# Optimization experiments

Hardware: AMD Instinct MI355X
Metric: run time of the kernel (lower is better)

The kernel has to match this reference:

```python
import jax, jax.numpy as jnp
import numpy as np

EPS = 1e-5

def _layer_norm(x, gamma, beta):
    # LayerNorm over the last two dims [C, 128], matching nn.LayerNorm([C, 128])
    mean = jnp.mean(x, axis=(-2, -1), keepdims=True)
    var = jnp.var(x, axis=(-2, -1), keepdims=True)
    return (x - mean) * jax.lax.rsqrt(var + EPS) * gamma + beta


def setup_inputs() -> dict:
    key = jax.random.key(0)
    ks = jax.random.split(key, 7)
    B, C, N, L = 64, 1024, 128, 512
    W_SCALE = 0.02  # keep pre-softmax logits / activations in a sane range
    return {
        "X_in": jax.random.normal(ks[0], (B, C, N), jnp.float32),
        "T": jax.random.normal(ks[1], (B, C, L), jnp.float32),
        "Wq": jax.random.normal(ks[2], (C, C), jnp.float32) * W_SCALE,
        "Wk": jax.random.normal(ks[3], (C, C), jnp.float32) * W_SCALE,
        "Wv": jax.random.normal(ks[4], (C, C), jnp.float32) * W_SCALE,
        "Wf1": jax.random.normal(ks[5], (C, C), jnp.float32) * W_SCALE,
        "Wf2": jax.random.normal(ks[6], (C, C), jnp.float32) * W_SCALE,
        "gamma": jnp.ones((C, N), jnp.float32),
        "beta": jnp.zeros((C, N), jnp.float32),
    }


def reference(X_in, T, Wq, Wk, Wv, Wf1, Wf2, gamma, beta):
    C = Wq.shape[1]  # feature_map_cs (intended value of the buggy X_in.weight.shape[1])
    # 1x1 Conv1d == per-position channel matmul: weight [out, in]
    q = jnp.einsum('oc,bcn->bon', Wq, X_in)      # [B, C, N]
    k = jnp.einsum('oc,bcl->bol', Wk, T)         # [B, C, L]
    sim = jnp.einsum('bcn,bcl->bnl', q, k) / jnp.sqrt(jnp.float32(C))  # [B, N, L]
    attn = jax.nn.softmax(sim, axis=2)           # softmax over tokens L
    v = jnp.einsum('oc,bcl->bol', Wv, T)         # [B, C, L]
    ctx = jnp.einsum('bcl,bnl->bcn', v, attn)    # [B, C, N] == bmm(values, attn^T)
    X_out = _layer_norm(X_in + ctx, gamma, beta)
    h = jax.nn.relu(jnp.einsum('oc,bcn->bon', Wf1, X_out))
    ffn = jnp.einsum('oc,bcn->bon', Wf2, h)
    return _layer_norm(X_out + ffn, gamma, beta)
```

## Files before the change

kernel.cpp:

```cpp
#include <hip/hip_runtime.h>


using bf16   = __bf16;
using bf16x4 = __attribute__((ext_vector_type(4))) __bf16;
using bf16x8 = __attribute__((ext_vector_type(8))) __bf16;
using f32x4  = __attribute__((ext_vector_type(4))) float;

static constexpr int  Bb = 64;
static constexpr int  Cc = 1024;
static constexpr int  Nn = 128;
static constexpr int  Ll = 512;
static constexpr long long PLANE = (long long)Cc * Nn;
static constexpr float INV_PLANE = 1.0f / 131072.0f;

__device__ __forceinline__ void gload_lds16(const void* g, void* l) {
    __builtin_amdgcn_global_load_lds(
        (__attribute__((address_space(1))) void*)g,
        (__attribute__((address_space(3))) void*)l,
        16, 0, 0);
}

__global__ void __launch_bounds__(256)
prep_all(const float* __restrict__ Wv, const float* __restrict__ Wf1,
         const float* __restrict__ Wf2, const float* __restrict__ Wq,
         const float* __restrict__ Wk, const float* __restrict__ X,
         const float* __restrict__ T,
         bf16* __restrict__ WvB, bf16* __restrict__ Wf1B, bf16* __restrict__ Wf2B,
         bf16* __restrict__ WqT, bf16* __restrict__ WkT,
         bf16* __restrict__ Xt, bf16* __restrict__ Tt, bf16* __restrict__ Tb) {
    __shared__ float tile[64][65];
    const int bx = blockIdx.x;
    const int t  = threadIdx.x;
    if (bx < 3072) {
        const float* in = bx < 1024 ? Wv : (bx < 2048 ? Wf1 : Wf2);
        bf16* out       = bx < 1024 ? WvB : (bx < 2048 ? Wf1B : Wf2B);
        int i = (bx & 1023) * 256 + t;
        float4 v = reinterpret_cast<const float4*>(in)[i];
        bf16x4 o = { (bf16)v.x, (bf16)v.y, (bf16)v.z, (bf16)v.w };
        reinterpret_cast<bf16x4*>(out)[i] = o;
        return;
    }
    const float* in; bf16* outT; bf16* outS = nullptr;
    int R, S, bxx, byy, bz = 0;
    if (bx < 3584) {
        int j = bx - 3072;
        in = (j >= 256) ? Wk : Wq; outT = (j >= 256) ? WkT : WqT;
        R = Cc; S = Cc; j &= 255; bxx = j & 15; byy = j >> 4;
    } else if (bx < 5632) {
        int j = bx - 3584; bz = j >> 5; j &= 31;
        bxx = j & 1; byy = j >> 1; in = X; outT = Xt; R = Cc; S = Nn;
    } else {
        int j = bx - 5632; bz = j >> 7; j &= 127;
        bxx = j & 7; byy = j >> 3; in = T; outT = Tt; outS = Tb; R = Cc; S = Ll;
    }
    long long plane = (long long)R * S;
    in   += (long long)bz * plane;
    outT += (long long)bz * plane;
    if (outS) outS += (long long)bz * plane;
    int s0 = bxx * 64, r0 = byy * 64;
    int rl = t >> 4;
    int sc = (t & 15) * 4;
    #pragma unroll
    for (int p = 0; p < 4; ++p) {
        int r = p * 16 + rl;
        float4 v = *(const float4*)(in + (long long)(r0 + r) * S + s0 + sc);
        *(float4*)&tile[r][sc] = v;
        if (outS) {
            bf16x4 o = { (bf16)v.x, (bf16)v.y, (bf16)v.z, (bf16)v.w };
            *(bf16x4*)(outS + (long long)(r0 + r) * S + s0 + sc) = o;
        }
    }
    __syncthreads();
    long long tb = ((long long)(s0 >> 6) * (R >> 6) + (r0 >> 6)) * 4096;
    int sb = t >> 3;
    int rg = (t & 7) * 8;
    #pragma unroll
    for (int p = 0; p < 2; ++p) {
        int s = sb + p * 32;
        bf16x8 o;
        #pragma unroll
        for (int j = 0; j < 8; ++j) o[j] = (bf16)tile[rg + j][s];
        *(bf16x8*)(outT + tb + s * 64 + rg) = o;
    }
}

#define GEMM_PROLOGUE_AND_LOOP(A_, Bt_, K_, TA_, TB_)                              \
    __shared__ bf16 As[2][128 * 64];                                               \
    __shared__ bf16 Bs[2][128 * 64];                                               \
    const int n0   = blockIdx.x * 128;                                             \
    const int m0   = blockIdx.y * 128;                                             \
    const int t    = threadIdx.x;                                                  \
    const int lane = t & 63;                                                       \
    const int w    = t >> 6;                                                       \
    const int wr   = (w >> 1) * 64;                                                \
    const int wc   = (w & 1) * 64;                                                 \
    const int lr   = lane & 15;                                                    \
    const int hi4  = (lane >> 4) * 16;                                             \
    const int sw   = (lr & 7) << 4;                                                \
    const int stepA_ = (TA_) ? 4096 : 64;                                          \
    const int stepB_ = (TB_) ? 4096 : 64;                                          \
    const bf16* gA[4]; const bf16* gB[4]; int lo[4];                               \
    _Pragma("unroll")                                                              \
    for (int p = 0; p < 4; ++p) {                                                  \
        int o = w * 1024 + lane * 16 + p * 4096;                                   \
        int row = o >> 7;                                                          \
        int scol = ((o & 127) ^ ((row & 7) << 4)) >> 1;                            \
        lo[p] = o;                                                                 \
        int ra = m0 + row, rb = n0 + row;                                          \
        gA[p] = (TA_) ? A_ + ((long long)(ra >> 6) * (K_ >> 6)) * 4096             \
                           + (ra & 63) * 64 + scol                                 \
                      : A_ + (long long)ra * K_ + scol;                            \
        gB[p] = (TB_) ? Bt_ + ((long long)(rb >> 6) * (K_ >> 6)) * 4096            \
                            + (rb & 63) * 64 + scol                                \
                      : Bt_ + (long long)rb * K_ + scol;                           \
    }                                                                              \
    f32x4 acc[4][4] = {};                                                          \
    const int NT_ = K_ / 64;                                                       \
    _Pragma("unroll")                                                              \
    for (int p = 0; p < 4; ++p) gload_lds16(gA[p], (char*)As[0] + lo[p]);          \
    _Pragma("unroll")                                                              \
    for (int p = 0; p < 4; ++p) gload_lds16(gB[p], (char*)Bs[0] + lo[p]);          \
    __syncthreads();                                                               \
    int cur_ = 0;                                                                  \
    for (int kt = 0; kt < NT_; ++kt) {                                             \
        if (kt + 1 < NT_) {                                                        \
            _Pragma("unroll")                                                      \
            for (int p = 0; p < 4; ++p)                                            \
                gload_lds16(gA[p] + (long long)(kt + 1) * stepA_,                  \
                            (char*)As[cur_ ^ 1] + lo[p]);                          \
            _Pragma("unroll")                                                      \
            for (int p = 0; p < 4; ++p)                                            \
                gload_lds16(gB[p] + (long long)(kt + 1) * stepB_,                  \
                            (char*)Bs[cur_ ^ 1] + lo[p]);                          \
        }                                                                          \
        const bf16* As_ = As[cur_]; const bf16* Bs_ = Bs[cur_];                    \
        _Pragma("unroll")                                                          \
        for (int kk = 0; kk < 2; ++kk) {                                           \
            bf16x8 af[4], bfr[4];                                                  \
            _Pragma("unroll")                                                      \
            for (int i = 0; i < 4; ++i) {                                          \
                int ra = wr + i * 16 + lr;                                         \
                int rb = wc + i * 16 + lr;                                         \
                af[i]  = *(const bf16x8*)((const char*)As_ +                       \
                          ((((ra << 7) + (kk << 6) + hi4)) ^ sw));                 \
                bfr[i] = *(const bf16x8*)((const char*)Bs_ +                       \
                          ((((rb << 7) + (kk << 6) + hi4)) ^ sw));                 \
            }                                                                      \
            _Pragma("unroll")                                                      \
            for (int mi = 0; mi < 4; ++mi)                                         \
                _Pragma("unroll")                                                  \
                for (int ni = 0; ni < 4; ++ni)                                     \
                    acc[mi][ni] = __builtin_amdgcn_mfma_f32_16x16x32_bf16(         \
                        af[mi], bfr[ni], acc[mi][ni], 0, 0, 0);                    \
        }                                                                          \
        __syncthreads();                                                           \
        cur_ ^= 1;                                                                 \
    }

template <typename OutT, bool RELU, int TA, int TB>
__global__ void __launch_bounds__(256, 2)
gemm_tn(const bf16* __restrict__ A, const bf16* __restrict__ Bt, OutT* __restrict__ C,
        int M, int N, int K, long long sA, long long sBt, long long sC, float scale) {
    A  += (long long)blockIdx.z * sA;
    Bt += (long long)blockIdx.z * sBt;
    C  += (long long)blockIdx.z * sC;
    GEMM_PROLOGUE_AND_LOOP(A, Bt, K, TA, TB)
    const int rbase = m0 + wr + (lane >> 4) * 4;
    const int cbase = n0 + wc + lr;
    #pragma unroll
    for (int mi = 0; mi < 4; ++mi)
        #pragma unroll
        for (int ni = 0; ni < 4; ++ni)
            #pragma unroll
            for (int r = 0; r < 4; ++r) {
                float v = acc[mi][ni][r] * scale;
                if (RELU) v = fmaxf(v, 0.0f);
                C[(long long)(rbase + mi * 16 + r) * N + (cbase + ni * 16)] = (OutT)v;
            }
}

__global__ void __launch_bounds__(256, 2)
gemm_sim_exp(const bf16* __restrict__ A , const bf16* __restrict__ Bt ,
             bf16* __restrict__ E, float* __restrict__ rspart, int K,
             long long sA, long long sBt) {
    A  += (long long)blockIdx.z * sA;
    Bt += (long long)blockIdx.z * sBt;
    E  += (long long)blockIdx.z * ((long long)Nn * Ll);
    GEMM_PROLOGUE_AND_LOOP(A, Bt, K, 0, 1)
    const int rbase = m0 + wr + (lane >> 4) * 4;
    const int cbase = n0 + wc + lr;
    __shared__ float rs[2][128];
    float psum[4][4];
    #pragma unroll
    for (int mi = 0; mi < 4; ++mi)
        #pragma unroll
        for (int r = 0; r < 4; ++r) psum[mi][r] = 0.f;
    #pragma unroll
    for (int mi = 0; mi < 4; ++mi)
        #pragma unroll
        for (int ni = 0; ni < 4; ++ni)
            #pragma unroll
            for (int r = 0; r < 4; ++r) {
                float ev = __expf(acc[mi][ni][r] * 0.03125f);
                E[(long long)(rbase + mi * 16 + r) * Ll + (cbase + ni * 16)] = (bf16)ev;
                psum[mi][r] += ev;
            }
    #pragma unroll
    for (int mi = 0; mi < 4; ++mi)
        #pragma unroll
        for (int r = 0; r < 4; ++r) {
            float v = psum[mi][r];
            v += __shfl_xor(v, 1); v += __shfl_xor(v, 2);
            v += __shfl_xor(v, 4); v += __shfl_xor(v, 8);
            psum[mi][r] = v;
        }
    if (lr == 0) {
        #pragma unroll
        for (int mi = 0; mi < 4; ++mi)
            #pragma unroll
            for (int r = 0; r < 4; ++r)
                rs[wc ? 1 : 0][wr + (lane >> 4) * 4 + mi * 16 + r] = psum[mi][r];
    }
    __syncthreads();
    if (t < 128)
        rspart[((long long)blockIdx.z * 4 + blockIdx.x) * 128 + t] = rs[0][t] + rs[1][t];
}

__global__ void __launch_bounds__(256, 2)
gemm_u_scaled(const bf16* __restrict__ A , const bf16* __restrict__ Bt ,
              bf16* __restrict__ C, const float* __restrict__ rspart, int K,
              long long sA, long long sBt, long long sC) {
    A  += (long long)blockIdx.z * sA;
    Bt += (long long)blockIdx.z * sBt;
    C  += (long long)blockIdx.z * sC;
    const float* rp = rspart + (long long)blockIdx.z * 512;
    GEMM_PROLOGUE_AND_LOOP(A, Bt, K, 0, 0)
    const int rbase = m0 + wr + (lane >> 4) * 4;
    const int cbase = n0 + wc + lr;
    #pragma unroll
    for (int mi = 0; mi < 4; ++mi)
        #pragma unroll
        for (int r = 0; r < 4; ++r) {
            int row = rbase + mi * 16 + r;
            float inv = 1.f / (rp[row] + rp[128 + row] + rp[256 + row] + rp[384 + row]);
            #pragma unroll
            for (int ni = 0; ni < 4; ++ni)
                C[(long long)row * Cc + (cbase + ni * 16)] = (bf16)(acc[mi][ni][r] * inv);
        }
}

__global__ void __launch_bounds__(256, 2)
gemm_ctx_ln1(const bf16* __restrict__ A , const bf16* __restrict__ Bt ,
             const float* __restrict__ X, bf16* __restrict__ Z1, float* __restrict__ partials,
             int K, long long sBt) {
    const int N = Nn;
    Bt += (long long)blockIdx.z * sBt;
    X  += (long long)blockIdx.z * PLANE;
    Z1 += (long long)blockIdx.z * PLANE;
    GEMM_PROLOGUE_AND_LOOP(A, Bt, K, 0, 0)
    const int rbase = m0 + wr + (lane >> 4) * 4;
    const int cbase = n0 + wc + lr;
    float s = 0.f, ss = 0.f;
    #pragma unroll
    for (int mi = 0; mi < 4; ++mi)
        #pragma unroll
        for (int ni = 0; ni < 4; ++ni)
            #pragma unroll
            for (int r = 0; r < 4; ++r) {
                long long idx = (long long)(rbase + mi * 16 + r) * N + (cbase + ni * 16);
                float zv = acc[mi][ni][r] + X[idx];
                Z1[idx] = (bf16)zv;
                s += zv; ss += zv * zv;
            }
    #pragma unroll
    for (int off = 32; off; off >>= 1) { s += __shfl_xor(s, off); ss += __shfl_xor(ss, off); }
    __shared__ float red[8];
    if (lane == 0) { red[w] = s; red[4 + w] = ss; }
    __syncthreads();
    if (t == 0) {
        float S = red[0] + red[1] + red[2] + red[3];
        float SS = red[4] + red[5] + red[6] + red[7];
        float* p = partials + ((long long)blockIdx.z * 8 + blockIdx.y) * 2;
        p[0] = S; p[1] = SS;
    }
}

__global__ void __launch_bounds__(256, 2)
gemm_ffn_ln2(const bf16* __restrict__ A , const bf16* __restrict__ Bt ,
             const bf16* __restrict__ Z1, const float* __restrict__ pp1,
             const float* __restrict__ gamma, const float* __restrict__ beta,
             bf16* __restrict__ Z2, float* __restrict__ partials,
             int K, long long sA) {
    A  += (long long)blockIdx.z * sA;
    Z1 += (long long)blockIdx.z * PLANE;
    Z2 += (long long)blockIdx.z * PLANE;
    float S1 = 0.f, SS1 = 0.f;
    #pragma unroll
    for (int j = 0; j < 8; ++j) {
        S1  += pp1[((long long)blockIdx.z * 8 + j) * 2];
        SS1 += pp1[((long long)blockIdx.z * 8 + j) * 2 + 1];
    }
    const float mean1 = S1 * INV_PLANE;
    const float rstd1 = rsqrtf(SS1 * INV_PLANE - mean1 * mean1 + 1e-5f);
    GEMM_PROLOGUE_AND_LOOP(A, Bt, K, 0, 0)
    const int rbase = m0 + wr + (lane >> 4) * 4;
    const int cbase = n0 + wc + lr;
    float s = 0.f, ss = 0.f;
    #pragma unroll
    for (int mi = 0; mi < 4; ++mi)
        #pragma unroll
        for (int ni = 0; ni < 4; ++ni) {
            long long a = (long long)(cbase + ni * 16) * Nn + rbase + mi * 16;
            bf16x4 z1v = *(const bf16x4*)(Z1 + a);
            float4 g  = *(const float4*)(gamma + a);
            float4 be = *(const float4*)(beta + a);
            float x0 = ((float)z1v[0] - mean1) * rstd1 * g.x + be.x;
            float x1 = ((float)z1v[1] - mean1) * rstd1 * g.y + be.y;
            float x2 = ((float)z1v[2] - mean1) * rstd1 * g.z + be.z;
            float x3 = ((float)z1v[3] - mean1) * rstd1 * g.w + be.w;
            float z0 = acc[mi][ni][0] + x0, z1 = acc[mi][ni][1] + x1;
            float z2 = acc[mi][ni][2] + x2, z3 = acc[mi][ni][3] + x3;
            bf16x4 zo = { (bf16)z0, (bf16)z1, (bf16)z2, (bf16)z3 };
            *(bf16x4*)(Z2 + a) = zo;
            s  += z0 + z1 + z2 + z3;
            ss += z0 * z0 + z1 * z1 + z2 * z2 + z3 * z3;
        }
    #pragma unroll
    for (int off = 32; off; off >>= 1) { s += __shfl_xor(s, off); ss += __shfl_xor(ss, off); }
    __shared__ float red[8];
    if (lane == 0) { red[w] = s; red[4 + w] = ss; }
    __syncthreads();
    if (t == 0) {
        float S = red[0] + red[1] + red[2] + red[3];
        float SS = red[4] + red[5] + red[6] + red[7];
        float* p = partials + ((long long)blockIdx.z * 8 + blockIdx.x) * 2;
        p[0] = S; p[1] = SS;
    }
}

__global__ void ln1_norm_transpose(const bf16* __restrict__ Z1, const float* __restrict__ partials,
                                   const float* __restrict__ gamma, const float* __restrict__ beta,
                                   bf16* __restrict__ XoutT) {
    int b = blockIdx.z;
    float S = 0.f, SS = 0.f;
    #pragma unroll
    for (int j = 0; j < 8; ++j) {
        S  += partials[((long long)b * 8 + j) * 2];
        SS += partials[((long long)b * 8 + j) * 2 + 1];
    }
    float mean = S * INV_PLANE;
    float var  = SS * INV_PLANE - mean * mean;
    float rstd = rsqrtf(var + 1e-5f);
    __shared__ float tile[64][65];
    long long base = (long long)b * PLANE;
    int n0 = blockIdx.x * 64, c0 = blockIdx.y * 64;
    int t = threadIdx.x;
    int rl = t >> 4;
    int sc = (t & 15) * 4;
    #pragma unroll
    for (int p = 0; p < 4; ++p) {
        int r = p * 16 + rl;
        long long idx = (long long)(c0 + r) * Nn + n0 + sc;
        bf16x4 z  = *(const bf16x4*)(Z1 + base + idx);
        float4 g  = *(const float4*)(gamma + idx);
        float4 be = *(const float4*)(beta + idx);
        float4 o = {((float)z[0] - mean) * rstd * g.x + be.x,
                    ((float)z[1] - mean) * rstd * g.y + be.y,
                    ((float)z[2] - mean) * rstd * g.z + be.z,
                    ((float)z[3] - mean) * rstd * g.w + be.w};
        *(float4*)&tile[r][sc] = o;
    }
    __syncthreads();
    long long tb = ((long long)(n0 >> 6) * (Cc >> 6) + (c0 >> 6)) * 4096;
    int sb = t >> 3;
    int rg = (t & 7) * 8;
    #pragma unroll
    for (int p = 0; p < 2; ++p) {
        int n = sb + p * 32;
        bf16x8 o;
        #pragma unroll
        for (int j = 0; j < 8; ++j) o[j] = (bf16)tile[rg + j][n];
        *(bf16x8*)(XoutT + base + tb + n * 64 + rg) = o;
    }
}

__global__ void ln2_final(const bf16* __restrict__ Z2, const float* __restrict__ partials,
                          const float* __restrict__ gamma, const float* __restrict__ beta,
                          float* __restrict__ out) {
    int b = blockIdx.y;
    float S = 0.f, SS = 0.f;
    #pragma unroll
    for (int j = 0; j < 8; ++j) {
        S  += partials[((long long)b * 8 + j) * 2];
        SS += partials[((long long)b * 8 + j) * 2 + 1];
    }
    float mean = S * INV_PLANE;
    float var  = SS * INV_PLANE - mean * mean;
    float rstd = rsqrtf(var + 1e-5f);
    long long base = (long long)b * PLANE;
    int i = (blockIdx.x * 256 + threadIdx.x) * 8;
    bf16x8 z = *(const bf16x8*)(Z2 + base + i);
    #pragma unroll
    for (int h = 0; h < 2; ++h) {
        float4 g  = *(const float4*)(gamma + i + h * 4);
        float4 be = *(const float4*)(beta + i + h * 4);
        float4 o = {((float)z[h * 4 + 0] - mean) * rstd * g.x + be.x,
                    ((float)z[h * 4 + 1] - mean) * rstd * g.y + be.y,
                    ((float)z[h * 4 + 2] - mean) * rstd * g.z + be.z,
                    ((float)z[h * 4 + 3] - mean) * rstd * g.w + be.w};
        *(float4*)(out + base + i + h * 4) = o;
    }
}

extern "C" void kernel_launch(void* const* d_in, const int* in_sizes, int n_in,
                              void* d_out, int out_size, void* d_ws, size_t ws_size,
                              hipStream_t stream) {
    const float* X   = (const float*)d_in[0];
    const float* T   = (const float*)d_in[1];
    const float* Wq  = (const float*)d_in[2];
    const float* Wk  = (const float*)d_in[3];
    const float* Wv  = (const float*)d_in[4];
    const float* Wf1 = (const float*)d_in[5];
    const float* Wf2 = (const float*)d_in[6];
    const float* gamma = (const float*)d_in[7];
    const float* beta  = (const float*)d_in[8];
    float* out = (float*)d_out;
    char* ws = (char*)d_ws;
    const size_t MB = 1ull << 20;

    bf16* WvB  = (bf16*)(ws + 0 * MB);
    bf16* Wf1B = (bf16*)(ws + 2 * MB);
    bf16* Wf2B = (bf16*)(ws + 4 * MB);
    bf16* WqT  = (bf16*)(ws + 6 * MB);
    bf16* WkT  = (bf16*)(ws + 8 * MB);
    bf16* G2   = (bf16*)(ws + 10 * MB);
    bf16* Xt   = (bf16*)(ws + 12 * MB);
    bf16* Tt   = (bf16*)(ws + 28 * MB);
    bf16* Z1   = (bf16*)(ws + 28 * MB);
    bf16* Tb   = (bf16*)(ws + 92 * MB);
    bf16* XoutT= (bf16*)(ws + 92 * MB);
    bf16* hT   = (bf16*)(ws + 108 * MB);
    bf16* e    = (bf16*)(ws + 156 * MB);
    bf16* Z2   = (bf16*)(ws + 156 * MB);
    bf16* E    = (bf16*)(ws + 188 * MB);
    bf16* u    = (bf16*)(ws + 196 * MB);
    float* pp1 = (float*)(ws + 212 * MB);
    float* pp2 = (float*)(ws + 212 * MB + 65536);
    float* rsp = (float*)(ws + 213 * MB);

    dim3 blk256(256);

    prep_all<<<dim3(13824), blk256, 0, stream>>>(
        Wv, Wf1, Wf2, Wq, Wk, X, T, WvB, Wf1B, Wf2B, WqT, WkT, Xt, Tt, Tb);

    gemm_tn<bf16, false, 1, 1><<<dim3(8, 8, 1), blk256, 0, stream>>>(
        WkT, WqT, G2, Cc, Cc, Cc, 0, 0, 0, 1.f);
    gemm_tn<bf16, false, 1, 0><<<dim3(8, 1, Bb), blk256, 0, stream>>>(
        Xt, G2, e, Nn, Cc, Cc, (long long)Nn * Cc, 0, (long long)Nn * Cc, 1.f);
    gemm_sim_exp<<<dim3(4, 1, Bb), blk256, 0, stream>>>(
        e, Tt, E, rsp, Cc, (long long)Nn * Cc, (long long)Ll * Cc);
    gemm_u_scaled<<<dim3(8, 1, Bb), blk256, 0, stream>>>(
        E, Tb, u, rsp, Ll, (long long)Nn * Ll, (long long)Cc * Ll, (long long)Nn * Cc);
    gemm_ctx_ln1<<<dim3(1, 8, Bb), blk256, 0, stream>>>(
        WvB, u, X, Z1, pp1, Cc, (long long)Nn * Cc);
    ln1_norm_transpose<<<dim3(Nn / 64, Cc / 64, Bb), blk256, 0, stream>>>(
        Z1, pp1, gamma, beta, XoutT);
    gemm_tn<bf16, true, 1, 0><<<dim3(8, 1, Bb), blk256, 0, stream>>>(
        XoutT, Wf1B, hT, Nn, Cc, Cc, (long long)Nn * Cc, 0, (long long)Nn * Cc, 1.f);
    gemm_ffn_ln2<<<dim3(8, 1, Bb), blk256, 0, stream>>>(
        hT, Wf2B, Z1, pp1, gamma, beta, Z2, pp2, Cc, (long long)Nn * Cc);
    ln2_final<<<dim3(64, Bb), blk256, 0, stream>>>(Z2, pp2, gamma, beta, out);
}
```

Measured before the change: 293.3 us.

## Fuse T fp32-to-bf16 conversion into attention GEMMs and split-K the G2 GEMM

Drops the separate pass that converted T into transposed and plain bf16 copies. The sim and context GEMMs now read fp32 T directly, converting it in registers (through an LDS transpose for the sim GEMM) while staging tiles. This removes a large write-then-read of bf16 T through HBM. The Wk^T·Wq GEMM is also split four ways along K into fp32 partials plus a small reduce kernel, giving it more blocks to run on. The cost is twice the global read bytes for T in each GEMM, extra LDS and sync work inside the main loops, and one extra kernel launch.

```diff
diff --git a/kernel.cpp b/kernel.cpp
--- a/kernel.cpp
+++ b/kernel.cpp
@@ -24,10 +24,8 @@
 prep_all(const float* __restrict__ Wv, const float* __restrict__ Wf1,
          const float* __restrict__ Wf2, const float* __restrict__ Wq,
          const float* __restrict__ Wk, const float* __restrict__ X,
-         const float* __restrict__ T,
          bf16* __restrict__ WvB, bf16* __restrict__ Wf1B, bf16* __restrict__ Wf2B,
-         bf16* __restrict__ WqT, bf16* __restrict__ WkT,
-         bf16* __restrict__ Xt, bf16* __restrict__ Tt, bf16* __restrict__ Tb) {
+         bf16* __restrict__ WqT, bf16* __restrict__ WkT, bf16* __restrict__ Xt) {
     __shared__ float tile[64][65];
     const int bx = blockIdx.x;
     const int t  = threadIdx.x;
@@ -40,40 +38,30 @@
         reinterpret_cast<bf16x4*>(out)[i] = o;
         return;
     }
-    const float* in; bf16* outT; bf16* outS = nullptr;
+    const float* in; bf16* outT;
     int R, S, bxx, byy, bz = 0;
     if (bx < 3584) {
         int j = bx - 3072;
         in = (j >= 256) ? Wk : Wq; outT = (j >= 256) ? WkT : WqT;
         R = Cc; S = Cc; j &= 255; bxx = j & 15; byy = j >> 4;
-    } else if (bx < 5632) {
+    } else {
         int j = bx - 3584; bz = j >> 5; j &= 31;
         bxx = j & 1; byy = j >> 1; in = X; outT = Xt; R = Cc; S = Nn;
-    } else {
-        int j = bx - 5632; bz = j >> 7; j &= 127;
-        bxx = j & 7; byy = j >> 3; in = T; outT = Tt; outS = Tb; R = Cc; S = Ll;
     }
     long long plane = (long long)R * S;
     in   += (long long)bz * plane;
     outT += (long long)bz * plane;
-    if (outS) outS += (long long)bz * plane;
     int s0 = bxx * 64, r0 = byy * 64;
-    int rl = t >> 4;
-    int sc = (t & 15) * 4;
+    int rl = t >> 4, sc = (t & 15) * 4;
     #pragma unroll
     for (int p = 0; p < 4; ++p) {
         int r = p * 16 + rl;
         float4 v = *(const float4*)(in + (long long)(r0 + r) * S + s0 + sc);
         *(float4*)&tile[r][sc] = v;
-        if (outS) {
-            bf16x4 o = { (bf16)v.x, (bf16)v.y, (bf16)v.z, (bf16)v.w };
-            *(bf16x4*)(outS + (long long)(r0 + r) * S + s0 + sc) = o;
-        }
     }
     __syncthreads();
     long long tb = ((long long)(s0 >> 6) * (R >> 6) + (r0 >> 6)) * 4096;
-    int sb = t >> 3;
-    int rg = (t & 7) * 8;
+    int sb = t >> 3, rg = (t & 7) * 8;
     #pragma unroll
     for (int p = 0; p < 2; ++p) {
         int s = sb + p * 32;
@@ -84,7 +72,7 @@
     }
 }
 
-#define GEMM_PROLOGUE_AND_LOOP(A_, Bt_, K_, TA_, TB_)                              \
+#define GEMM_PROLOGUE_AND_LOOP(A_, Bt_, KLOOP_, LD_, TA_, TB_)                     \
     __shared__ bf16 As[2][128 * 64];                                               \
     __shared__ bf16 Bs[2][128 * 64];                                               \
     const int n0   = blockIdx.x * 128;                                             \
@@ -107,15 +95,15 @@
         int scol = ((o & 127) ^ ((row & 7) << 4)) >> 1;                            \
         lo[p] = o;                                                                 \
         int ra = m0 + row, rb = n0 + row;                                          \
-        gA[p] = (TA_) ? A_ + ((long long)(ra >> 6) * (K_ >> 6)) * 4096             \
+        gA[p] = (TA_) ? A_ + ((long long)(ra >> 6) * (LD_ >> 6)) * 4096            \
                            + (ra & 63) * 64 + scol                                 \
-                      : A_ + (long long)ra * K_ + scol;                            \
-        gB[p] = (TB_) ? Bt_ + ((long long)(rb >> 6) * (K_ >> 6)) * 4096            \
+                      : A_ + (long long)ra * LD_ + scol;                           \
+        gB[p] = (TB_) ? Bt_ + ((long long)(rb >> 6) * (LD_ >> 6)) * 4096           \
                             + (rb & 63) * 64 + scol                                \
-                      : Bt_ + (long long)rb * K_ + scol;                           \
+                      : Bt_ + (long long)rb * LD_ + scol;                          \
     }                                                                              \
     f32x4 acc[4][4] = {};                                                          \
-    const int NT_ = K_ / 64;                                                       \
+    const int NT_ = KLOOP_ / 64;                                                   \
     _Pragma("unroll")                                                              \
     for (int p = 0; p < 4; ++p) gload_lds16(gA[p], (char*)As[0] + lo[p]);          \
     _Pragma("unroll")                                                              \
@@ -160,11 +148,12 @@
 template <typename OutT, bool RELU, int TA, int TB>
 __global__ void __launch_bounds__(256, 2)
 gemm_tn(const bf16* __restrict__ A, const bf16* __restrict__ Bt, OutT* __restrict__ C,
-        int M, int N, int K, long long sA, long long sBt, long long sC, float scale) {
+        int M, int N, int KLOOP, int ld, long long sA, long long sBt, long long sC,
+        float scale) {
     A  += (long long)blockIdx.z * sA;
     Bt += (long long)blockIdx.z * sBt;
     C  += (long long)blockIdx.z * sC;
-    GEMM_PROLOGUE_AND_LOOP(A, Bt, K, TA, TB)
+    GEMM_PROLOGUE_AND_LOOP(A, Bt, KLOOP, ld, TA, TB)
     const int rbase = m0 + wr + (lane >> 4) * 4;
     const int cbase = n0 + wc + lr;
     #pragma unroll
@@ -179,17 +168,100 @@
             }
 }
 
+__global__ void g2_reduce(const float* __restrict__ p, bf16* __restrict__ g2) {
+    int i = (blockIdx.x * 256 + threadIdx.x) * 4;
+    float4 a = *(const float4*)(p + i);
+    float4 b = *(const float4*)(p + 1048576 + i);
+    float4 c = *(const float4*)(p + 2097152 + i);
+    float4 d = *(const float4*)(p + 3145728 + i);
+    bf16x4 o = { (bf16)(a.x + b.x + c.x + d.x), (bf16)(a.y + b.y + c.y + d.y),
+                 (bf16)(a.z + b.z + c.z + d.z), (bf16)(a.w + b.w + c.w + d.w) };
+    *(bf16x4*)(g2 + i) = o;
+}
+
 __global__ void __launch_bounds__(256, 2)
-gemm_sim_exp(const bf16* __restrict__ A , const bf16* __restrict__ Bt ,
-             bf16* __restrict__ E, float* __restrict__ rspart, int K,
-             long long sA, long long sBt) {
-    A  += (long long)blockIdx.z * sA;
-    Bt += (long long)blockIdx.z * sBt;
+gemm_sim_exp(const bf16* __restrict__ A , const float* __restrict__ Tg,
+             bf16* __restrict__ E, float* __restrict__ rspart) {
+    __shared__ char smem[49152];
+    __shared__ float scratch[64 * 132];
+    __shared__ float rs[2][128];
+    bf16* AsB = (bf16*)smem;
+    bf16* Bs  = (bf16*)(smem + 32768);
+    A  += (long long)blockIdx.z * ((long long)Nn * Cc);
+    Tg += (long long)blockIdx.z * ((long long)Cc * Ll);
     E  += (long long)blockIdx.z * ((long long)Nn * Ll);
-    GEMM_PROLOGUE_AND_LOOP(A, Bt, K, 0, 1)
-    const int rbase = m0 + wr + (lane >> 4) * 4;
+    const int n0 = blockIdx.x * 128;
+    const int t = threadIdx.x, lane = t & 63, w = t >> 6;
+    const int wr = (w >> 1) * 64, wc = (w & 1) * 64;
+    const int lr = lane & 15, hi4 = (lane >> 4) * 16, sw = (lr & 7) << 4;
+    const bf16* gA[4]; int lo[4];
+    #pragma unroll
+    for (int p = 0; p < 4; ++p) {
+        int o = w * 1024 + lane * 16 + p * 4096;
+        int row = o >> 7;
+        int scol = ((o & 127) ^ ((row & 7) << 4)) >> 1;
+        lo[p] = o;
+        gA[p] = A + (long long)row * Cc + scol;
+    }
+    const int s1_rc = t >> 2, s1_l = (t & 3) * 32;
+    const int s2_l = t & 127, s2_ch = (t >> 7) * 8;
+    float4 treg[8];
+    #pragma unroll
+    for (int p = 0; p < 4; ++p) gload_lds16(gA[p], (char*)AsB + lo[p]);
+    #pragma unroll
+    for (int i = 0; i < 8; ++i)
+        treg[i] = *(const float4*)(Tg + (long long)s1_rc * Ll + n0 + s1_l + i * 4);
+    f32x4 acc[4][4] = {};
+    int cur = 0;
+    const int NT = Cc / 64;
+    for (int kt = 0; kt < NT; ++kt) {
+        if (kt + 1 < NT) {
+            #pragma unroll
+            for (int p = 0; p < 4; ++p)
+                gload_lds16(gA[p] + (kt + 1) * 64, (char*)AsB + (cur ^ 1) * 16384 + lo[p]);
+        }
+        #pragma unroll
+        for (int i = 0; i < 8; ++i)
+            *(float4*)&scratch[s1_rc * 132 + s1_l + i * 4] = treg[i];
+        __syncthreads();
+        if (kt + 1 < NT) {
+            #pragma unroll
+            for (int i = 0; i < 8; ++i)
+                treg[i] = *(const float4*)(Tg + (long long)((kt + 1) * 64 + s1_rc) * Ll
+                                           + n0 + s1_l + i * 4);
+        }
+        #pragma unroll
+        for (int g = 0; g < 4; ++g) {
+            int c0 = s2_ch + g * 16;
+            bf16x8 bv;
+            #pragma unroll
+            for (int j = 0; j < 8; ++j) bv[j] = (bf16)scratch[(c0 + j) * 132 + s2_l];
+            *(bf16x8*)((char*)Bs + ((s2_l * 128 + c0 * 2) ^ ((s2_l & 7) << 4))) = bv;
+        }
+        __syncthreads();
+        const bf16* As_ = AsB + cur * 8192;
+        #pragma unroll
+        for (int kk = 0; kk < 2; ++kk) {
+            bf16x8 af[4], bfr[4];
+            #pragma unroll
+            for (int i = 0; i < 4; ++i) {
+                int ra = wr + i * 16 + lr;
+                int rb = wc + i * 16 + lr;
+                af[i]  = *(const bf16x8*)((const char*)As_ + (((ra << 7) + (kk << 6) + hi4) ^ sw));
+                bfr[i] = *(const bf16x8*)((const char*)Bs  + (((rb << 7) + (kk << 6) + hi4) ^ sw));
+            }
+            #pragma unroll
+            for (int mi = 0; mi < 4; ++mi)
+                #pragma unroll
+                for (int ni = 0; ni < 4; ++ni)
+                    acc[mi][ni] = __builtin_amdgcn_mfma_f32_16x16x32_bf16(
+                        af[mi], bfr[ni], acc[mi][ni], 0, 0, 0);
+        }
+        __syncthreads();
+        cur ^= 1;
+    }
+    const int rbase = wr + (lane >> 4) * 4;
     const int cbase = n0 + wc + lr;
-    __shared__ float rs[2][128];
     float psum[4][4];
     #pragma unroll
     for (int mi = 0; mi < 4; ++mi)
@@ -227,15 +299,83 @@
 }
 
 __global__ void __launch_bounds__(256, 2)
-gemm_u_scaled(const bf16* __restrict__ A , const bf16* __restrict__ Bt ,
-              bf16* __restrict__ C, const float* __restrict__ rspart, int K,
-              long long sA, long long sBt, long long sC) {
-    A  += (long long)blockIdx.z * sA;
-    Bt += (long long)blockIdx.z * sBt;
-    C  += (long long)blockIdx.z * sC;
+gemm_u_scaled(const bf16* __restrict__ A , const float* __restrict__ Tg,
+              bf16* __restrict__ C, const float* __restrict__ rspart) {
+    __shared__ char smem[49152];
+    bf16* AsB = (bf16*)smem;
+    bf16* Bs  = (bf16*)(smem + 32768);
+    A  += (long long)blockIdx.z * ((long long)Nn * Ll);
+    Tg += (long long)blockIdx.z * ((long long)Cc * Ll);
+    C  += (long long)blockIdx.z * ((long long)Nn * Cc);
     const float* rp = rspart + (long long)blockIdx.z * 512;
-    GEMM_PROLOGUE_AND_LOOP(A, Bt, K, 0, 0)
-    const int rbase = m0 + wr + (lane >> 4) * 4;
+    const int n0 = blockIdx.x * 128;
+    const int t = threadIdx.x, lane = t & 63, w = t >> 6;
+    const int wr = (w >> 1) * 64, wc = (w & 1) * 64;
+    const int lr = lane & 15, hi4 = (lane >> 4) * 16, sw = (lr & 7) << 4;
+    const bf16* gA[4]; int lo[4];
+    #pragma unroll
+    for (int p = 0; p < 4; ++p) {
+        int o = w * 1024 + lane * 16 + p * 4096;
+        int row = o >> 7;
+        int scol = ((o & 127) ^ ((row & 7) << 4)) >> 1;
+        lo[p] = o;
+        gA[p] = A + (long long)row * Ll + scol;
+    }
+    const int s_c = t >> 1, s_half = (t & 1) * 32;
+    float4 treg[8];
+    #pragma unroll
+    for (int p = 0; p < 4; ++p) gload_lds16(gA[p], (char*)AsB + lo[p]);
+    #pragma unroll
+    for (int i = 0; i < 8; ++i)
+        treg[i] = *(const float4*)(Tg + (long long)(n0 + s_c) * Ll + s_half + i * 4);
+    f32x4 acc[4][4] = {};
+    int cur = 0;
+    const int NT = Ll / 64;
+    for (int kt = 0; kt < NT; ++kt) {
+        if (kt + 1 < NT) {
+            #pragma unroll
+            for (int p = 0; p < 4; ++p)
+                gload_lds16(gA[p] + (kt + 1) * 64, (char*)AsB + (cur ^ 1) * 16384 + lo[p]);
+        }
+        __syncthreads();
+        #pragma unroll
+        for (int q = 0; q < 4; ++q) {
+            bf16x8 bv;
+            #pragma unroll
+            for (int j = 0; j < 4; ++j) {
+                bv[j]     = (bf16)((const float*)&treg[q * 2])[j];
+                bv[4 + j] = (bf16)((const float*)&treg[q * 2 + 1])[j];
+            }
+            *(bf16x8*)((char*)Bs + ((s_c * 128 + (s_half + q * 8) * 2) ^ ((s_c & 7) << 4))) = bv;
+        }
+        if (kt + 1 < NT) {
+            #pragma unroll
+            for (int i = 0; i < 8; ++i)
+                treg[i] = *(const float4*)(Tg + (long long)(n0 + s_c) * Ll
+                                           + (kt + 1) * 64 + s_half + i * 4);
+        }
+        __syncthreads();
+        const bf16* As_ = AsB + cur * 8192;
+        #pragma unroll
+        for (int kk = 0; kk < 2; ++kk) {
+            bf16x8 af[4], bfr[4];
+            #pragma unroll
+            for (int i = 0; i < 4; ++i) {
+                int ra = wr + i * 16 + lr;
+                int rb = wc + i * 16 + lr;
+                af[i]  = *(const bf16x8*)((const char*)As_ + (((ra << 7) + (kk << 6) + hi4) ^ sw));
+                bfr[i] = *(const bf16x8*)((const char*)Bs  + (((rb << 7) + (kk << 6) + hi4) ^ sw));
+            }
+            #pragma unroll
+            for (int mi = 0; mi < 4; ++mi)
+                #pragma unroll
+                for (int ni = 0; ni < 4; ++ni)
+                    acc[mi][ni] = __builtin_amdgcn_mfma_f32_16x16x32_bf16(
+                        af[mi], bfr[ni], acc[mi][ni], 0, 0, 0);
+        }
+        cur ^= 1;
+    }
+    const int rbase = wr + (lane >> 4) * 4;
     const int cbase = n0 + wc + lr;
     #pragma unroll
     for (int mi = 0; mi < 4; ++mi)
@@ -257,7 +397,7 @@
     Bt += (long long)blockIdx.z * sBt;
     X  += (long long)blockIdx.z * PLANE;
     Z1 += (long long)blockIdx.z * PLANE;
-    GEMM_PROLOGUE_AND_LOOP(A, Bt, K, 0, 0)
+    GEMM_PROLOGUE_AND_LOOP(A, Bt, K, K, 0, 0)
     const int rbase = m0 + wr + (lane >> 4) * 4;
     const int cbase = n0 + wc + lr;
     float s = 0.f, ss = 0.f;
@@ -302,7 +442,7 @@
     }
     const float mean1 = S1 * INV_PLANE;
     const float rstd1 = rsqrtf(SS1 * INV_PLANE - mean1 * mean1 + 1e-5f);
-    GEMM_PROLOGUE_AND_LOOP(A, Bt, K, 0, 0)
+    GEMM_PROLOGUE_AND_LOOP(A, Bt, K, K, 0, 0)
     const int rbase = m0 + wr + (lane >> 4) * 4;
     const int cbase = n0 + wc + lr;
     float s = 0.f, ss = 0.f;
@@ -349,14 +489,12 @@
         SS += partials[((long long)b * 8 + j) * 2 + 1];
     }
     float mean = S * INV_PLANE;
-    float var  = SS * INV_PLANE - mean * mean;
-    float rstd = rsqrtf(var + 1e-5f);
+    float rstd = rsqrtf(SS * INV_PLANE - mean * mean + 1e-5f);
     __shared__ float tile[64][65];
     long long base = (long long)b * PLANE;
     int n0 = blockIdx.x * 64, c0 = blockIdx.y * 64;
     int t = threadIdx.x;
-    int rl = t >> 4;
-    int sc = (t & 15) * 4;
+    int rl = t >> 4, sc = (t & 15) * 4;
     #pragma unroll
     for (int p = 0; p < 4; ++p) {
         int r = p * 16 + rl;
@@ -372,8 +510,7 @@
     }
     __syncthreads();
     long long tb = ((long long)(n0 >> 6) * (Cc >> 6) + (c0 >> 6)) * 4096;
-    int sb = t >> 3;
-    int rg = (t & 7) * 8;
+    int sb = t >> 3, rg = (t & 7) * 8;
     #pragma unroll
     for (int p = 0; p < 2; ++p) {
         int n = sb + p * 32;
@@ -395,8 +532,7 @@
         SS += partials[((long long)b * 8 + j) * 2 + 1];
     }
     float mean = S * INV_PLANE;
-    float var  = SS * INV_PLANE - mean * mean;
-    float rstd = rsqrtf(var + 1e-5f);
+    float rstd = rsqrtf(SS * INV_PLANE - mean * mean + 1e-5f);
     long long base = (long long)b * PLANE;
     int i = (blockIdx.x * 256 + threadIdx.x) * 8;
     bf16x8 z = *(const bf16x8*)(Z2 + base + i);
@@ -435,38 +571,37 @@
     bf16* WkT  = (bf16*)(ws + 8 * MB);
     bf16* G2   = (bf16*)(ws + 10 * MB);
     bf16* Xt   = (bf16*)(ws + 12 * MB);
-    bf16* Tt   = (bf16*)(ws + 28 * MB);
     bf16* Z1   = (bf16*)(ws + 28 * MB);
-    bf16* Tb   = (bf16*)(ws + 92 * MB);
-    bf16* XoutT= (bf16*)(ws + 92 * MB);
-    bf16* hT   = (bf16*)(ws + 108 * MB);
-    bf16* e    = (bf16*)(ws + 156 * MB);
-    bf16* Z2   = (bf16*)(ws + 156 * MB);
-    bf16* E    = (bf16*)(ws + 188 * MB);
-    bf16* u    = (bf16*)(ws + 196 * MB);
-    float* pp1 = (float*)(ws + 212 * MB);
-    float* pp2 = (float*)(ws + 212 * MB + 65536);
-    float* rsp = (float*)(ws + 213 * MB);
+    bf16* XoutT= (bf16*)(ws + 44 * MB);
+    bf16* hT   = (bf16*)(ws + 60 * MB);
+    bf16* e    = (bf16*)(ws + 76 * MB);
+    bf16* Z2   = (bf16*)(ws + 92 * MB);
+    bf16* E    = (bf16*)(ws + 108 * MB);
+    bf16* u    = (bf16*)(ws + 116 * MB);
+    float* G2p = (float*)(ws + 132 * MB);
+    float* pp1 = (float*)(ws + 148 * MB);
+    float* pp2 = (float*)(ws + 148 * MB + 65536);
+    float* rsp = (float*)(ws + 149 * MB);
 
     dim3 blk256(256);
 
-    prep_all<<<dim3(13824), blk256, 0, stream>>>(
-        Wv, Wf1, Wf2, Wq, Wk, X, T, WvB, Wf1B, Wf2B, WqT, WkT, Xt, Tt, Tb);
-
-    gemm_tn<bf16, false, 1, 1><<<dim3(8, 8, 1), blk256, 0, stream>>>(
-        WkT, WqT, G2, Cc, Cc, Cc, 0, 0, 0, 1.f);
+    prep_all<<<dim3(5632), blk256, 0, stream>>>(
+        Wv, Wf1, Wf2, Wq, Wk, X, WvB, Wf1B, Wf2B, WqT, WkT, Xt);
+
+    gemm_tn<float, false, 1, 1><<<dim3(8, 8, 4), blk256, 0, stream>>>(
+        WkT, WqT, G2p, Cc, Cc, 256, Cc, 16384, 16384, 1048576, 1.f);
+    g2_reduce<<<dim3(1024), blk256, 0, stream>>>(G2p, G2);
+
     gemm_tn<bf16, false, 1, 0><<<dim3(8, 1, Bb), blk256, 0, stream>>>(
-        Xt, G2, e, Nn, Cc, Cc, (long long)Nn * Cc, 0, (long long)Nn * Cc, 1.f);
-    gemm_sim_exp<<<dim3(4, 1, Bb), blk256, 0, stream>>>(
-        e, Tt, E, rsp, Cc, (long long)Nn * Cc, (long long)Ll * Cc);
-    gemm_u_scaled<<<dim3(8, 1, Bb), blk256, 0, stream>>>(
-        E, Tb, u, rsp, Ll, (long long)Nn * Ll, (long long)Cc * Ll, (long long)Nn * Cc);
+        Xt, G2, e, Nn, Cc, Cc, Cc, (long long)Nn * Cc, 0, (long long)Nn * Cc, 1.f);
+    gemm_sim_exp<<<dim3(4, 1, Bb), blk256, 0, stream>>>(e, T, E, rsp);
+    gemm_u_scaled<<<dim3(8, 1, Bb), blk256, 0, stream>>>(E, T, u, rsp);
     gemm_ctx_ln1<<<dim3(1, 8, Bb), blk256, 0, stream>>>(
         WvB, u, X, Z1, pp1, Cc, (long long)Nn * Cc);
     ln1_norm_transpose<<<dim3(Nn / 64, Cc / 64, Bb), blk256, 0, stream>>>(
         Z1, pp1, gamma, beta, XoutT);
     gemm_tn<bf16, true, 1, 0><<<dim3(8, 1, Bb), blk256, 0, stream>>>(
-        XoutT, Wf1B, hT, Nn, Cc, Cc, (long long)Nn * Cc, 0, (long long)Nn * Cc, 1.f);
+        XoutT, Wf1B, hT, Nn, Cc, Cc, Cc, (long long)Nn * Cc, 0, (long long)Nn * Cc, 1.f);
     gemm_ffn_ln2<<<dim3(8, 1, Bb), blk256, 0, stream>>>(
         hT, Wf2B, Z1, pp1, gamma, beta, Z2, pp2, Cc, (long long)Nn * Cc);
     ln2_final<<<dim3(64, Bb), blk256, 0, stream>>>(Z2, pp2, gamma, beta, out);
```

Result: faster. 285.6 us (-2.6%).
